# Kernel tuning notes

Measured on AMD Instinct MI355X. Metric: run time of the kernel, lower is better.

The kernel has to match this reference:

```python
import jax, jax.numpy as jnp
import numpy as np

N_NODES = 20000
N_EDGES = 320000
N_GRAPHS = 128
IN_CH = 64
DIM = 32
NEG_SLOPE = 0.2
EPS = 1e-16


def _gat_conv(x, src, dst, W, att_src, att_dst, bias, heads, ch):
    """PyG GATConv (concat=True, self-loops already included in src/dst).
    x: [N, F_in]; W: [heads*ch, F_in]; att_*: [heads, ch]; bias: [heads*ch].
    Returns [N, heads*ch]."""
    N = x.shape[0]
    h = (x @ W.T).reshape(N, heads, ch)                      # [N, H, C]
    a_src = (h * att_src[None]).sum(-1)                      # [N, H]
    a_dst = (h * att_dst[None]).sum(-1)                      # [N, H]
    e = jax.nn.leaky_relu(a_src[src] + a_dst[dst], NEG_SLOPE)  # [E, H]
    # segment softmax over edges sharing a destination node
    m = jax.ops.segment_max(e, dst, num_segments=N)          # [N, H]
    ex = jnp.exp(e - m[dst])
    s = jax.ops.segment_sum(ex, dst, num_segments=N)
    alpha = ex / (s[dst] + EPS)                              # [E, H]
    msg = alpha[:, :, None] * h[src]                         # [E, H, C]
    out = jax.ops.segment_sum(msg, dst, num_segments=N)      # [N, H, C]
    return out.reshape(N, heads * ch) + bias[None, :]


def setup_inputs() -> dict:
    key = jax.random.key(0)
    ks = jax.random.split(key, 20)

    x = jax.random.normal(ks[0], (N_NODES, IN_CH), dtype=jnp.float32)
    edge_index = jax.random.randint(ks[1], (2, N_EDGES), 0, N_NODES, dtype=jnp.int64)
    batch = jnp.sort(jax.random.randint(ks[2], (N_NODES,), 0, N_GRAPHS, dtype=jnp.int64))

    def lin_init(k, shape, fan_in):
        return jax.random.normal(k, shape, dtype=jnp.float32) * (1.0 / np.sqrt(fan_in))

    H1, C1 = 5, DIM * 2      # conv1: in -> dim*2, heads 5 -> out dim*10
    H2, C2 = 5, DIM * 3      # conv2: dim*10 -> dim*3, heads 5 -> out dim*15
    H3, C3 = 1, DIM          # conv3: dim*15 -> dim, heads 1

    inp = {
        "x": x,
        "W1": lin_init(ks[3], (H1 * C1, IN_CH), IN_CH),
        "att_src1": lin_init(ks[4], (H1, C1), C1),
        "att_dst1": lin_init(ks[5], (H1, C1), C1),
        "b1": jnp.zeros((H1 * C1,), jnp.float32),
        "W2": lin_init(ks[6], (H2 * C2, H1 * C1), H1 * C1),
        "att_src2": lin_init(ks[7], (H2, C2), C2),
        "att_dst2": lin_init(ks[8], (H2, C2), C2),
        "b2": jnp.zeros((H2 * C2,), jnp.float32),
        "W3": lin_init(ks[9], (H3 * C3, H2 * C2), H2 * C2),
        "att_src3": lin_init(ks[10], (H3, C3), C3),
        "att_dst3": lin_init(ks[11], (H3, C3), C3),
        "b3": jnp.zeros((H3 * C3,), jnp.float32),
        "lin_w": lin_init(ks[12], (1024, DIM), DIM),
        "lin_b": jnp.zeros((1024,), jnp.float32),
        "lin2_w": lin_init(ks[13], (1, 1024), 1024),
        "lin2_b": jnp.zeros((1,), jnp.float32),
        "edge_index": edge_index,
        "batch": batch,
    }
    return inp


def reference(x, W1, att_src1, att_dst1, b1,
              W2, att_src2, att_dst2, b2,
              W3, att_src3, att_dst3, b3,
              lin_w, lin_b, lin2_w, lin2_b,
              edge_index, batch):
    N = x.shape[0]
    # PyG GATConv adds self-loops by default
    loops = jnp.arange(N, dtype=edge_index.dtype)
    src = jnp.concatenate([edge_index[0], loops])
    dst = jnp.concatenate([edge_index[1], loops])

    h = _gat_conv(x, src, dst, W1, att_src1, att_dst1, b1, 5, DIM * 2)
    h = jax.nn.relu(h)                                   # dropout p=0 -> identity
    h = _gat_conv(h, src, dst, W2, att_src2, att_dst2, b2, 5, DIM * 3)
    h = jax.nn.relu(h)
    h = _gat_conv(h, src, dst, W3, att_src3, att_dst3, b3, 1, DIM)
    h = jax.nn.relu(h)

    g = jax.ops.segment_sum(h, batch, num_segments=N_GRAPHS)   # global_add_pool [G, dim]
    g = jax.nn.relu(g @ lin_w.T + lin_b[None, :])
    g = g @ lin2_w.T + lin2_b[None, :]
    return jax.nn.sigmoid(g)                                   # [G, out_channels]
```

## Files before the change

kernel.cpp:

```cpp
#include <hip/hip_runtime.h>
#include <math.h>

#define NN 20000
#define NE 320000
#define NG 128

typedef short short8 __attribute__((ext_vector_type(8)));
typedef float f32x4 __attribute__((ext_vector_type(4)));
typedef float f32x2 __attribute__((ext_vector_type(2)));
typedef unsigned short ushort;
typedef unsigned short ushort4v __attribute__((ext_vector_type(4)));
typedef float float4v __attribute__((ext_vector_type(4)));
typedef unsigned int uint;
typedef unsigned int uint2v __attribute__((ext_vector_type(2)));

__device__ __forceinline__ float b2f(ushort u) {
    unsigned int v = ((unsigned int)u) << 16;
    return __uint_as_float(v);
}
__device__ __forceinline__ ushort f2b(float f) {
    unsigned int u = __float_as_uint(f);
    u = (u + 0x7fff + ((u >> 16) & 1)) >> 16;
    return (ushort)u;
}
__device__ __forceinline__ float lrelu(float x) { return x >= 0.f ? x : 0.2f * x; }
__device__ __forceinline__ unsigned char f2f8(float v) {
    return (unsigned char)(__builtin_amdgcn_cvt_pk_fp8_f32(v, v, 0, false) & 0xff);
}
__device__ __forceinline__ void dec8(uint2v r, f32x2 d[4]) {
    d[0] = __builtin_amdgcn_cvt_pk_f32_fp8(r.x, false);
    d[1] = __builtin_amdgcn_cvt_pk_f32_fp8(r.x, true);
    d[2] = __builtin_amdgcn_cvt_pk_f32_fp8(r.y, false);
    d[3] = __builtin_amdgcn_cvt_pk_f32_fp8(r.y, true);
}

#define CVT_N0 (NN * 64 / 4)
#define CVT_N1 (320 * 64 / 4)
#define CVT_N2 (480 * 320 / 4)
#define CVT_N3 (32 * 480 / 4)
__global__ void f2b4_kernel(const float* __restrict__ a0, ushort* __restrict__ o0,
                            const float* __restrict__ a1, ushort* __restrict__ o1,
                            const float* __restrict__ a2, ushort* __restrict__ o2,
                            const float* __restrict__ a3, ushort* __restrict__ o3) {
    int i = blockIdx.x * blockDim.x + threadIdx.x;
    const float* src; ushort* dst; int li;
    if (i < CVT_N0) { src = a0; dst = o0; li = i; }
    else if (i < CVT_N0 + CVT_N1) { src = a1; dst = o1; li = i - CVT_N0; }
    else if (i < CVT_N0 + CVT_N1 + CVT_N2) { src = a2; dst = o2; li = i - CVT_N0 - CVT_N1; }
    else if (i < CVT_N0 + CVT_N1 + CVT_N2 + CVT_N3) { src = a3; dst = o3; li = i - CVT_N0 - CVT_N1 - CVT_N2; }
    else return;
    float4v v = *(const float4v*)(src + (size_t)li * 4);
    ushort4v r;
    r.x = f2b(v.x); r.y = f2b(v.y); r.z = f2b(v.z); r.w = f2b(v.w);
    *(ushort4v*)(dst + (size_t)li * 4) = r;
}

__global__ void count_kernel(const int* __restrict__ dst, int* __restrict__ cnt, int E) {
    int i = blockIdx.x * blockDim.x + threadIdx.x;
    if (i < E) atomicAdd(&cnt[dst[i]], 1);
}

__global__ __launch_bounds__(1024) void scan_kernel(const int* __restrict__ cnt,
                                                    int* __restrict__ row_start, int n) {
    __shared__ int sh[1024];
    int tid = threadIdx.x;
    int base = tid * 20;
    int local[20];
    int s = 0;
    #pragma unroll
    for (int k = 0; k < 20; ++k) {
        int idx = base + k;
        int v = (idx < n) ? cnt[idx] : 0;
        local[k] = s;
        s += v;
    }
    sh[tid] = s;
    __syncthreads();
    for (int off = 1; off < 1024; off <<= 1) {
        int t = (tid >= off) ? sh[tid - off] : 0;
        __syncthreads();
        sh[tid] += t;
        __syncthreads();
    }
    int pre = (tid == 0) ? 0 : sh[tid - 1];
    #pragma unroll
    for (int k = 0; k < 20; ++k) {
        int idx = base + k;
        if (idx < n) row_start[idx] = pre + local[k];
    }
    if (tid == 1023) row_start[n] = sh[1023];
}

__global__ void fill_kernel(const int* __restrict__ src, const int* __restrict__ dst,
                            const int* __restrict__ row_start, int* __restrict__ cursor,
                            int* __restrict__ csr_src, int E) {
    int i = blockIdx.x * blockDim.x + threadIdx.x;
    if (i < E) {
        int d = dst[i];
        int pos = atomicAdd(&cursor[d], 1);
        csr_src[row_start[d] + pos] = src[i];
    }
}

template <int K, int NF, int H, bool F8>
__global__ __launch_bounds__(256) void gemm_lds(const ushort* __restrict__ A,
                                                const ushort* __restrict__ B,
                                                ushort* __restrict__ C,
                                                unsigned char* __restrict__ C8,
                                                const float* __restrict__ att_src,
                                                const float* __restrict__ att_dst,
                                                float* __restrict__ a_src,
                                                float* __restrict__ a_dst,
                                                int M, int N, int gridx) {
    constexpr int BN = NF * 16;
    constexpr int KP = K + 8;
    constexpr int KS = K / 32;
    __shared__ ushort Bs[BN][KP];

    const int nwg = gridDim.x;
    int bid = blockIdx.x;
    {
        int q = nwg >> 3, r = nwg & 7;
        int xcd = bid & 7, idx = bid >> 3;
        bid = (xcd < r ? xcd * (q + 1) : r * (q + 1) + (xcd - r) * q) + idx;
    }
    const int by = bid / gridx;
    const int bx = bid % gridx;
    const int bn = bx * BN;

    const int tid = threadIdx.x;
    const int w = tid >> 6;
    const int lane = tid & 63;
    const int l15 = lane & 15;
    const int lhi = lane >> 4;

    constexpr int NCH = BN * (K / 8);
    for (int i = tid; i < NCH; i += 256) {
        int r = i / (K / 8), c8 = i % (K / 8);
        short8 v = *(const short8*)(B + (size_t)(bn + r) * K + c8 * 8);
        *(short8*)(&Bs[r][c8 * 8]) = v;
    }
    __syncthreads();

    const int bm = by * 64 + w * 16;
    int arow = bm + l15;
    if (arow >= M) arow = M - 1;
    const ushort* ap = A + (size_t)arow * K + lhi * 8;

    f32x4 acc[NF];
    #pragma unroll
    for (int f = 0; f < NF; ++f) acc[f] = (f32x4){0.f, 0.f, 0.f, 0.f};

    short8 a_cur = *(const short8*)ap;
    short8 b_cur[NF], b_nxt[NF];
    #pragma unroll
    for (int f = 0; f < NF; ++f)
        b_cur[f] = *(const short8*)(&Bs[f * 16 + l15][lhi * 8]);

    #pragma unroll
    for (int ks = 0; ks < KS; ++ks) {
        short8 a_nxt = a_cur;
        if (ks + 1 < KS) {
            a_nxt = *(const short8*)(ap + (ks + 1) * 32);
            #pragma unroll
            for (int f = 0; f < NF; ++f)
                b_nxt[f] = *(const short8*)(&Bs[f * 16 + l15][(ks + 1) * 32 + lhi * 8]);
        }
        #pragma unroll
        for (int f = 0; f < NF; ++f)
            acc[f] = __builtin_amdgcn_mfma_f32_16x16x32_bf16(a_cur, b_cur[f], acc[f], 0, 0, 0);
        a_cur = a_nxt;
        #pragma unroll
        for (int f = 0; f < NF; ++f) b_cur[f] = b_nxt[f];
    }

    #pragma unroll
    for (int f = 0; f < NF; ++f) {
        #pragma unroll
        for (int j = 0; j < 4; ++j) {
            int row = bm + lhi * 4 + j;
            if (row < M) {
                if (F8) C8[(size_t)row * N + bn + f * 16 + l15] = f2f8(acc[f][j]);
                else    C[(size_t)row * N + bn + f * 16 + l15] = f2b(acc[f][j]);
            }
        }
    }

    float as_v[NF], ad_v[NF];
    #pragma unroll
    for (int f = 0; f < NF; ++f) {
        as_v[f] = att_src[bx * BN + f * 16 + l15];
        ad_v[f] = att_dst[bx * BN + f * 16 + l15];
    }
    #pragma unroll
    for (int j = 0; j < 4; ++j) {
        float ps = 0.f, pd = 0.f;
        #pragma unroll
        for (int f = 0; f < NF; ++f) {
            ps += acc[f][j] * as_v[f];
            pd += acc[f][j] * ad_v[f];
        }
        #pragma unroll
        for (int off = 1; off < 16; off <<= 1) {
            ps += __shfl_xor(ps, off);
            pd += __shfl_xor(pd, off);
        }
        int row = bm + lhi * 4 + j;
        if (l15 == 0 && row < M) {
            a_src[row * H + bx] = ps;
            a_dst[row * H + bx] = pd;
        }
    }
}

template <int H, int C>
__global__ void gat_agg_f8(const unsigned char* __restrict__ h8,
                           const float* __restrict__ a_src, const float* __restrict__ a_dst,
                           const int* __restrict__ row_start, const int* __restrict__ csr_src,
                           const float* __restrict__ bias, ushort* __restrict__ out, int N) {
    constexpr int W = H * C;
    constexpr int VL = W / 8;
    int n = (blockIdx.x * blockDim.x + threadIdx.x) >> 6;
    int lane = threadIdx.x & 63;
    if (n >= N) return;
    bool act = lane < VL;
    int l = act ? lane : 0;
    int hd = (8 * l) / C;
    float adst = a_dst[n * H + hd];

    float m = lrelu(a_src[n * H + hd] + adst);
    float ssum = 1.f;
    f32x2 acc2[4];
    {
        uint2v r = *(const uint2v*)(h8 + (size_t)n * W + 8 * l);
        dec8(r, acc2);
    }

    int rs = row_start[n], re = row_start[n + 1];
    int i = rs;
    for (; i + 4 <= re; i += 4) {
        int s0 = csr_src[i], s1 = csr_src[i + 1], s2 = csr_src[i + 2], s3 = csr_src[i + 3];
        uint2v r0 = *(const uint2v*)(h8 + (size_t)s0 * W + 8 * l);
        uint2v r1 = *(const uint2v*)(h8 + (size_t)s1 * W + 8 * l);
        uint2v r2 = *(const uint2v*)(h8 + (size_t)s2 * W + 8 * l);
        uint2v r3 = *(const uint2v*)(h8 + (size_t)s3 * W + 8 * l);
        float e0 = lrelu(a_src[s0 * H + hd] + adst);
        float e1 = lrelu(a_src[s1 * H + hd] + adst);
        float e2 = lrelu(a_src[s2 * H + hd] + adst);
        float e3 = lrelu(a_src[s3 * H + hd] + adst);
        float nm = fmaxf(fmaxf(fmaxf(e0, e1), fmaxf(e2, e3)), m);
        float scale = __expf(m - nm);
        m = nm;
        float w0 = __expf(e0 - m), w1 = __expf(e1 - m);
        float w2 = __expf(e2 - m), w3 = __expf(e3 - m);
        ssum = ssum * scale + ((w0 + w1) + (w2 + w3));
        f32x2 d0[4], d1[4], d2[4], d3[4];
        dec8(r0, d0); dec8(r1, d1); dec8(r2, d2); dec8(r3, d3);
        f32x2 sc = {scale, scale};
        f32x2 vw0 = {w0, w0}, vw1 = {w1, w1}, vw2 = {w2, w2}, vw3 = {w3, w3};
        #pragma unroll
        for (int d = 0; d < 4; ++d) {
            f32x2 t = acc2[d] * sc;
            t += vw0 * d0[d];
            t += vw1 * d1[d];
            t += vw2 * d2[d];
            t += vw3 * d3[d];
            acc2[d] = t;
        }
    }
    for (; i < re; ++i) {
        int s = csr_src[i];
        uint2v r = *(const uint2v*)(h8 + (size_t)s * W + 8 * l);
        float e = lrelu(a_src[s * H + hd] + adst);
        float nm = fmaxf(m, e);
        float scale = __expf(m - nm);
        m = nm;
        float wgt = __expf(e - nm);
        ssum = ssum * scale + wgt;
        f32x2 dd[4];
        dec8(r, dd);
        f32x2 sc = {scale, scale};
        f32x2 vw = {wgt, wgt};
        #pragma unroll
        for (int d = 0; d < 4; ++d) acc2[d] = acc2[d] * sc + vw * dd[d];
    }

    float inv = 1.f / (ssum + 1e-16f);
    if (act) {
        short8 o;
        #pragma unroll
        for (int d = 0; d < 4; ++d) {
            #pragma unroll
            for (int e = 0; e < 2; ++e) {
                float v = acc2[d][e] * inv + bias[8 * l + 2 * d + e];
                o[2 * d + e] = (short)f2b(v > 0.f ? v : 0.f);
            }
        }
        *(short8*)(out + (size_t)n * W + 8 * l) = o;
    }
}

__global__ void gat_agg_c32(const ushort* __restrict__ h, const float* __restrict__ a_src,
                            const float* __restrict__ a_dst, const int* __restrict__ row_start,
                            const int* __restrict__ csr_src, const float* __restrict__ bias,
                            ushort* __restrict__ out, int N) {
    int n = (blockIdx.x * blockDim.x + threadIdx.x) >> 6;
    int lane = threadIdx.x & 63;
    if (n >= N) return;
    int g = lane >> 2;
    int q = lane & 3;
    float adst = a_dst[n];
    int rs = row_start[n];
    int total = row_start[n + 1] - rs + 1;

    float m = -1e30f, ssum = 0.f;
    float acc[8];
    #pragma unroll
    for (int j = 0; j < 8; ++j) acc[j] = 0.f;

    for (int k = g; k < total; k += 16) {
        int s = (k == 0) ? n : csr_src[rs + k - 1];
        float e = lrelu(a_src[s] + adst);
        float nm = fmaxf(m, e);
        float scale = __expf(m - nm);
        m = nm;
        float w = __expf(e - nm);
        ssum = ssum * scale + w;
        short8 r = *(const short8*)(h + (size_t)s * 32 + 8 * q);
        #pragma unroll
        for (int j = 0; j < 8; ++j) acc[j] = acc[j] * scale + w * b2f((ushort)r[j]);
    }

    #pragma unroll
    for (int off = 4; off < 64; off <<= 1) {
        float m2 = __shfl_xor(m, off);
        float s2 = __shfl_xor(ssum, off);
        float nm = fmaxf(m, m2);
        float sc1 = __expf(m - nm), sc2 = __expf(m2 - nm);
        ssum = ssum * sc1 + s2 * sc2;
        #pragma unroll
        for (int j = 0; j < 8; ++j) {
            float a2 = __shfl_xor(acc[j], off);
            acc[j] = acc[j] * sc1 + a2 * sc2;
        }
        m = nm;
    }

    if (lane < 4) {
        float inv = 1.f / (ssum + 1e-16f);
        short8 o;
        #pragma unroll
        for (int j = 0; j < 8; ++j) {
            float v = acc[j] * inv + bias[8 * lane + j];
            o[j] = (short)f2b(v > 0.f ? v : 0.f);
        }
        *(short8*)(out + (size_t)n * 32 + 8 * lane) = o;
    }
}

__global__ void pool_kernel(const ushort* __restrict__ x, const int* __restrict__ batch,
                            float* __restrict__ g, int N) {
    int wid = (blockIdx.x * blockDim.x + threadIdx.x) >> 6;
    int lane = threadIdx.x & 63;
    int node = wid * 2 + (lane >> 5);
    if (node >= N) return;
    int c = lane & 31;
    int b = batch[node];
    atomicAdd(&g[b * 32 + c], b2f(x[(size_t)node * 32 + c]));
}

__global__ void mlp1_kernel(const float* __restrict__ g, const float* __restrict__ w,
                            const float* __restrict__ b, float* __restrict__ hid) {
    int idx = blockIdx.x * blockDim.x + threadIdx.x;
    if (idx >= NG * 1024) return;
    int gr = idx >> 10, o = idx & 1023;
    float s = b[o];
    const float* gp = g + gr * 32;
    const float* wp = w + o * 32;
    #pragma unroll
    for (int k = 0; k < 32; ++k) s += gp[k] * wp[k];
    hid[idx] = s > 0.f ? s : 0.f;
}

__global__ void mlp2_kernel(const float* __restrict__ hid, const float* __restrict__ w2,
                            const float* __restrict__ b2, float* __restrict__ outp) {
    int wid = (blockIdx.x * blockDim.x + threadIdx.x) >> 6;
    int lane = threadIdx.x & 63;
    if (wid >= NG) return;
    float s = 0.f;
    for (int k = lane; k < 1024; k += 64) s += hid[wid * 1024 + k] * w2[k];
    for (int off = 32; off; off >>= 1) s += __shfl_down(s, off);
    if (lane == 0) outp[wid] = 1.f / (1.f + expf(-(s + b2[0])));
}

static inline size_t al256(size_t x) { return (x + 255) & ~(size_t)255; }

extern "C" void kernel_launch(void* const* d_in, const int* in_sizes, int n_in,
                              void* d_out, int out_size, void* d_ws, size_t ws_size,
                              hipStream_t stream) {
    const float* x      = (const float*)d_in[0];
    const float* W1     = (const float*)d_in[1];
    const float* as1    = (const float*)d_in[2];
    const float* ad1    = (const float*)d_in[3];
    const float* b1     = (const float*)d_in[4];
    const float* W2     = (const float*)d_in[5];
    const float* as2    = (const float*)d_in[6];
    const float* ad2    = (const float*)d_in[7];
    const float* b2     = (const float*)d_in[8];
    const float* W3     = (const float*)d_in[9];
    const float* as3    = (const float*)d_in[10];
    const float* ad3    = (const float*)d_in[11];
    const float* b3     = (const float*)d_in[12];
    const float* lin_w  = (const float*)d_in[13];
    const float* lin_b  = (const float*)d_in[14];
    const float* lin2_w = (const float*)d_in[15];
    const float* lin2_b = (const float*)d_in[16];
    const int*   ei     = (const int*)d_in[17];
    const int*   batch  = (const int*)d_in[18];
    float* outp = (float*)d_out;

    const int E = in_sizes[17] / 2;
    const int* e_src = ei;
    const int* e_dst = ei + E;

    char* p = (char*)d_ws;
    ushort* h_bf   = (ushort*)p; p += al256((size_t)NN * 480 * 2);
    ushort* o_bf   = (ushort*)p; p += al256((size_t)NN * 480 * 2);
    unsigned char* h_f8 = (unsigned char*)p; p += al256((size_t)NN * 480);
    ushort* x_bf   = (ushort*)p; p += al256((size_t)NN * 64 * 2);
    ushort* w1_bf  = (ushort*)p; p += al256((size_t)320 * 64 * 2);
    ushort* w2_bf  = (ushort*)p; p += al256((size_t)480 * 320 * 2);
    ushort* w3_bf  = (ushort*)p; p += al256((size_t)32 * 480 * 2);
    float* asrc    = (float*)p; p += al256((size_t)NN * 5 * 4);
    float* adst    = (float*)p; p += al256((size_t)NN * 5 * 4);
    int*   row_st  = (int*)p;   p += al256((size_t)(NN + 1) * 4);
    int*   cnt     = (int*)p;   p += al256((size_t)NN * 4);
    int*   csr_src = (int*)p;   p += al256((size_t)NE * 4);
    float* gpool   = (float*)p; p += al256((size_t)NG * 32 * 4);
    float* hidden  = (float*)p; p += al256((size_t)NG * 1024 * 4);
    (void)ws_size; (void)n_in; (void)out_size;

    dim3 blk(256);

    hipMemsetAsync(cnt, 0, NN * 4, stream);
    count_kernel<<<(E + 255) / 256, 256, 0, stream>>>(e_dst, cnt, E);
    scan_kernel<<<1, 1024, 0, stream>>>(cnt, row_st, NN);
    hipMemsetAsync(cnt, 0, NN * 4, stream);
    fill_kernel<<<(E + 255) / 256, 256, 0, stream>>>(e_src, e_dst, row_st, cnt, csr_src, E);

    {
        int tot = CVT_N0 + CVT_N1 + CVT_N2 + CVT_N3;
        f2b4_kernel<<<(tot + 255) / 256, blk, 0, stream>>>(x, x_bf, W1, w1_bf, W2, w2_bf, W3, w3_bf);
    }

    const int MPAN = (NN + 63) / 64;
    const int NBLK = (NN + 3) / 4;
    {
        gemm_lds<64, 4, 5, true><<<5 * MPAN, blk, 0, stream>>>(x_bf, w1_bf, h_bf, h_f8, as1, ad1, asrc, adst, NN, 320, 5);
        gat_agg_f8<5, 64><<<NBLK, blk, 0, stream>>>(h_f8, asrc, adst, row_st, csr_src, b1, o_bf, NN);
    }
    {
        gemm_lds<320, 6, 5, true><<<5 * MPAN, blk, 0, stream>>>(o_bf, w2_bf, h_bf, h_f8, as2, ad2, asrc, adst, NN, 480, 5);
        gat_agg_f8<5, 96><<<NBLK, blk, 0, stream>>>(h_f8, asrc, adst, row_st, csr_src, b2, o_bf, NN);
    }
    {
        gemm_lds<480, 2, 1, false><<<1 * MPAN, blk, 0, stream>>>(o_bf, w3_bf, h_bf, h_f8, as3, ad3, asrc, adst, NN, 32, 1);
        gat_agg_c32<<<NBLK, blk, 0, stream>>>(h_bf, asrc, adst, row_st, csr_src, b3, o_bf, NN);
    }
    hipMemsetAsync(gpool, 0, NG * 32 * 4, stream);
    pool_kernel<<<(NN / 2 * 64 + 255) / 256, blk, 0, stream>>>(o_bf, batch, gpool, NN);
    mlp1_kernel<<<(NG * 1024 + 255) / 256, blk, 0, stream>>>(gpool, lin_w, lin_b, hidden);
    mlp2_kernel<<<(NG * 64 + 255) / 256, blk, 0, stream>>>(hidden, lin2_w, lin2_b, outp);
}
```

Measured before the change: 212.1 us.

## Fuse pooling into last aggregation, merge MLP kernels, chunk GEMM B tiles

```diff
diff --git a/kernel.cpp b/kernel.cpp
--- a/kernel.cpp
+++ b/kernel.cpp
@@ -41,8 +41,13 @@
 __global__ void f2b4_kernel(const float* __restrict__ a0, ushort* __restrict__ o0,
                             const float* __restrict__ a1, ushort* __restrict__ o1,
                             const float* __restrict__ a2, ushort* __restrict__ o2,
-                            const float* __restrict__ a3, ushort* __restrict__ o3) {
+                            const float* __restrict__ a3, ushort* __restrict__ o3,
+                            float* __restrict__ gpool) {
     int i = blockIdx.x * blockDim.x + threadIdx.x;
+    if (i < NG * 32 / 4) {
+        float4v z = {0.f, 0.f, 0.f, 0.f};
+        *(float4v*)(gpool + (size_t)i * 4) = z;
+    }
     const float* src; ushort* dst; int li;
     if (i < CVT_N0) { src = a0; dst = o0; li = i; }
     else if (i < CVT_N0 + CVT_N1) { src = a1; dst = o1; li = i - CVT_N0; }
@@ -113,9 +118,10 @@
                                                 float* __restrict__ a_dst,
                                                 int M, int N, int gridx) {
     constexpr int BN = NF * 16;
-    constexpr int KP = K + 8;
-    constexpr int KS = K / 32;
-    __shared__ ushort Bs[BN][KP];
+    constexpr int KC = (K % 160 == 0) ? 160 : K;
+    constexpr int NCHK = K / KC;
+    constexpr int KS = KC / 32;
+    __shared__ ushort Bs[BN][KC + 8];
 
     const int nwg = gridDim.x;
     int bid = blockIdx.x;
@@ -134,14 +140,6 @@
     const int l15 = lane & 15;
     const int lhi = lane >> 4;
 
-    constexpr int NCH = BN * (K / 8);
-    for (int i = tid; i < NCH; i += 256) {
-        int r = i / (K / 8), c8 = i % (K / 8);
-        short8 v = *(const short8*)(B + (size_t)(bn + r) * K + c8 * 8);
-        *(short8*)(&Bs[r][c8 * 8]) = v;
-    }
-    __syncthreads();
-
     const int bm = by * 64 + w * 16;
     int arow = bm + l15;
     if (arow >= M) arow = M - 1;
@@ -151,27 +149,40 @@
     #pragma unroll
     for (int f = 0; f < NF; ++f) acc[f] = (f32x4){0.f, 0.f, 0.f, 0.f};
 
-    short8 a_cur = *(const short8*)ap;
-    short8 b_cur[NF], b_nxt[NF];
-    #pragma unroll
-    for (int f = 0; f < NF; ++f)
-        b_cur[f] = *(const short8*)(&Bs[f * 16 + l15][lhi * 8]);
-
-    #pragma unroll
-    for (int ks = 0; ks < KS; ++ks) {
-        short8 a_nxt = a_cur;
-        if (ks + 1 < KS) {
-            a_nxt = *(const short8*)(ap + (ks + 1) * 32);
+    #pragma unroll
+    for (int ch = 0; ch < NCHK; ++ch) {
+        const int c0 = ch * KC;
+        if (ch > 0) __syncthreads();
+        constexpr int NCH = BN * (KC / 8);
+        for (int i = tid; i < NCH; i += 256) {
+            int r = i / (KC / 8), c8 = i % (KC / 8);
+            short8 v = *(const short8*)(B + (size_t)(bn + r) * K + c0 + c8 * 8);
+            *(short8*)(&Bs[r][c8 * 8]) = v;
+        }
+        __syncthreads();
+
+        short8 a_cur = *(const short8*)(ap + c0);
+        short8 b_cur[NF], b_nxt[NF];
+        #pragma unroll
+        for (int f = 0; f < NF; ++f)
+            b_cur[f] = *(const short8*)(&Bs[f * 16 + l15][lhi * 8]);
+
+        #pragma unroll
+        for (int ks = 0; ks < KS; ++ks) {
+            short8 a_nxt = a_cur;
+            if (ks + 1 < KS) {
+                a_nxt = *(const short8*)(ap + c0 + (ks + 1) * 32);
+                #pragma unroll
+                for (int f = 0; f < NF; ++f)
+                    b_nxt[f] = *(const short8*)(&Bs[f * 16 + l15][(ks + 1) * 32 + lhi * 8]);
+            }
             #pragma unroll
             for (int f = 0; f < NF; ++f)
-                b_nxt[f] = *(const short8*)(&Bs[f * 16 + l15][(ks + 1) * 32 + lhi * 8]);
-        }
-        #pragma unroll
-        for (int f = 0; f < NF; ++f)
-            acc[f] = __builtin_amdgcn_mfma_f32_16x16x32_bf16(a_cur, b_cur[f], acc[f], 0, 0, 0);
-        a_cur = a_nxt;
-        #pragma unroll
-        for (int f = 0; f < NF; ++f) b_cur[f] = b_nxt[f];
+                acc[f] = __builtin_amdgcn_mfma_f32_16x16x32_bf16(a_cur, b_cur[f], acc[f], 0, 0, 0);
+            a_cur = a_nxt;
+            #pragma unroll
+            for (int f = 0; f < NF; ++f) b_cur[f] = b_nxt[f];
+        }
     }
 
     #pragma unroll
@@ -238,35 +249,65 @@
 
     int rs = row_start[n], re = row_start[n + 1];
     int i = rs;
-    for (; i + 4 <= re; i += 4) {
-        int s0 = csr_src[i], s1 = csr_src[i + 1], s2 = csr_src[i + 2], s3 = csr_src[i + 3];
-        uint2v r0 = *(const uint2v*)(h8 + (size_t)s0 * W + 8 * l);
-        uint2v r1 = *(const uint2v*)(h8 + (size_t)s1 * W + 8 * l);
-        uint2v r2 = *(const uint2v*)(h8 + (size_t)s2 * W + 8 * l);
-        uint2v r3 = *(const uint2v*)(h8 + (size_t)s3 * W + 8 * l);
-        float e0 = lrelu(a_src[s0 * H + hd] + adst);
-        float e1 = lrelu(a_src[s1 * H + hd] + adst);
-        float e2 = lrelu(a_src[s2 * H + hd] + adst);
-        float e3 = lrelu(a_src[s3 * H + hd] + adst);
-        float nm = fmaxf(fmaxf(fmaxf(e0, e1), fmaxf(e2, e3)), m);
+    for (; i + 8 <= re; i += 8) {
+        int s[8]; uint2v r[8]; float e[8];
+        #pragma unroll
+        for (int j = 0; j < 8; ++j) s[j] = csr_src[i + j];
+        #pragma unroll
+        for (int j = 0; j < 8; ++j) r[j] = *(const uint2v*)(h8 + (size_t)s[j] * W + 8 * l);
+        #pragma unroll
+        for (int j = 0; j < 8; ++j) e[j] = lrelu(a_src[s[j] * H + hd] + adst);
+        float nm = m;
+        #pragma unroll
+        for (int j = 0; j < 8; ++j) nm = fmaxf(nm, e[j]);
         float scale = __expf(m - nm);
         m = nm;
-        float w0 = __expf(e0 - m), w1 = __expf(e1 - m);
-        float w2 = __expf(e2 - m), w3 = __expf(e3 - m);
-        ssum = ssum * scale + ((w0 + w1) + (w2 + w3));
-        f32x2 d0[4], d1[4], d2[4], d3[4];
-        dec8(r0, d0); dec8(r1, d1); dec8(r2, d2); dec8(r3, d3);
         f32x2 sc = {scale, scale};
-        f32x2 vw0 = {w0, w0}, vw1 = {w1, w1}, vw2 = {w2, w2}, vw3 = {w3, w3};
-        #pragma unroll
-        for (int d = 0; d < 4; ++d) {
-            f32x2 t = acc2[d] * sc;
-            t += vw0 * d0[d];
-            t += vw1 * d1[d];
-            t += vw2 * d2[d];
-            t += vw3 * d3[d];
-            acc2[d] = t;
-        }
+        #pragma unroll
+        for (int d = 0; d < 4; ++d) acc2[d] *= sc;
+        ssum *= scale;
+        float wsum = 0.f;
+        #pragma unroll
+        for (int j = 0; j < 8; ++j) {
+            float wj = __expf(e[j] - nm);
+            wsum += wj;
+            f32x2 dd[4];
+            dec8(r[j], dd);
+            f32x2 vw = {wj, wj};
+            #pragma unroll
+            for (int d = 0; d < 4; ++d) acc2[d] += vw * dd[d];
+        }
+        ssum += wsum;
+    }
+    for (; i + 4 <= re; i += 4) {
+        int s[4]; uint2v r[4]; float e[4];
+        #pragma unroll
+        for (int j = 0; j < 4; ++j) s[j] = csr_src[i + j];
+        #pragma unroll
+        for (int j = 0; j < 4; ++j) r[j] = *(const uint2v*)(h8 + (size_t)s[j] * W + 8 * l);
+        #pragma unroll
+        for (int j = 0; j < 4; ++j) e[j] = lrelu(a_src[s[j] * H + hd] + adst);
+        float nm = m;
+        #pragma unroll
+        for (int j = 0; j < 4; ++j) nm = fmaxf(nm, e[j]);
+        float scale = __expf(m - nm);
+        m = nm;
+        f32x2 sc = {scale, scale};
+        #pragma unroll
+        for (int d = 0; d < 4; ++d) acc2[d] *= sc;
+        ssum *= scale;
+        float wsum = 0.f;
+        #pragma unroll
+        for (int j = 0; j < 4; ++j) {
+            float wj = __expf(e[j] - nm);
+            wsum += wj;
+            f32x2 dd[4];
+            dec8(r[j], dd);
+            f32x2 vw = {wj, wj};
+            #pragma unroll
+            for (int d = 0; d < 4; ++d) acc2[d] += vw * dd[d];
+        }
+        ssum += wsum;
     }
     for (; i < re; ++i) {
         int s = csr_src[i];
@@ -291,19 +332,19 @@
         #pragma unroll
         for (int d = 0; d < 4; ++d) {
             #pragma unroll
-            for (int e = 0; e < 2; ++e) {
-                float v = acc2[d][e] * inv + bias[8 * l + 2 * d + e];
-                o[2 * d + e] = (short)f2b(v > 0.f ? v : 0.f);
+            for (int e2 = 0; e2 < 2; ++e2) {
+                float v = acc2[d][e2] * inv + bias[8 * l + 2 * d + e2];
+                o[2 * d + e2] = (short)f2b(v > 0.f ? v : 0.f);
             }
         }
         *(short8*)(out + (size_t)n * W + 8 * l) = o;
     }
 }
 
-__global__ void gat_agg_c32(const ushort* __restrict__ h, const float* __restrict__ a_src,
-                            const float* __restrict__ a_dst, const int* __restrict__ row_start,
-                            const int* __restrict__ csr_src, const float* __restrict__ bias,
-                            ushort* __restrict__ out, int N) {
+__global__ void gat_agg_c32_pool(const ushort* __restrict__ h, const float* __restrict__ a_src,
+                                 const float* __restrict__ a_dst, const int* __restrict__ row_start,
+                                 const int* __restrict__ csr_src, const float* __restrict__ bias,
+                                 const int* __restrict__ batch, float* __restrict__ gpool, int N) {
     int n = (blockIdx.x * blockDim.x + threadIdx.x) >> 6;
     int lane = threadIdx.x & 63;
     if (n >= N) return;
@@ -348,49 +389,51 @@
 
     if (lane < 4) {
         float inv = 1.f / (ssum + 1e-16f);
-        short8 o;
+        int b = batch[n];
         #pragma unroll
         for (int j = 0; j < 8; ++j) {
             float v = acc[j] * inv + bias[8 * lane + j];
-            o[j] = (short)f2b(v > 0.f ? v : 0.f);
-        }
-        *(short8*)(out + (size_t)n * 32 + 8 * lane) = o;
-    }
-}
-
-__global__ void pool_kernel(const ushort* __restrict__ x, const int* __restrict__ batch,
-                            float* __restrict__ g, int N) {
-    int wid = (blockIdx.x * blockDim.x + threadIdx.x) >> 6;
-    int lane = threadIdx.x & 63;
-    int node = wid * 2 + (lane >> 5);
-    if (node >= N) return;
-    int c = lane & 31;
-    int b = batch[node];
-    atomicAdd(&g[b * 32 + c], b2f(x[(size_t)node * 32 + c]));
-}
-
-__global__ void mlp1_kernel(const float* __restrict__ g, const float* __restrict__ w,
-                            const float* __restrict__ b, float* __restrict__ hid) {
-    int idx = blockIdx.x * blockDim.x + threadIdx.x;
-    if (idx >= NG * 1024) return;
-    int gr = idx >> 10, o = idx & 1023;
-    float s = b[o];
-    const float* gp = g + gr * 32;
-    const float* wp = w + o * 32;
-    #pragma unroll
-    for (int k = 0; k < 32; ++k) s += gp[k] * wp[k];
-    hid[idx] = s > 0.f ? s : 0.f;
-}
-
-__global__ void mlp2_kernel(const float* __restrict__ hid, const float* __restrict__ w2,
-                            const float* __restrict__ b2, float* __restrict__ outp) {
-    int wid = (blockIdx.x * blockDim.x + threadIdx.x) >> 6;
-    int lane = threadIdx.x & 63;
-    if (wid >= NG) return;
-    float s = 0.f;
-    for (int k = lane; k < 1024; k += 64) s += hid[wid * 1024 + k] * w2[k];
-    for (int off = 32; off; off >>= 1) s += __shfl_down(s, off);
-    if (lane == 0) outp[wid] = 1.f / (1.f + expf(-(s + b2[0])));
+            v = v > 0.f ? v : 0.f;
+            atomicAdd(&gpool[b * 32 + 8 * lane + j], v);
+        }
+    }
+}
+
+__global__ __launch_bounds__(256) void mlp_fused(const float* __restrict__ gpool,
+                                                 const float* __restrict__ lin_w,
+                                                 const float* __restrict__ lin_b,
+                                                 const float* __restrict__ lin2_w,
+                                                 const float* __restrict__ lin2_b,
+                                                 float* __restrict__ outp) {
+    int gr = blockIdx.x;
+    int tid = threadIdx.x;
+    __shared__ float grow[32];
+    __shared__ float red[4];
+    if (tid < 8) {
+        float4v v = *(const float4v*)(gpool + gr * 32 + tid * 4);
+        *(float4v*)(&grow[tid * 4]) = v;
+    }
+    __syncthreads();
+    float partial = 0.f;
+    #pragma unroll
+    for (int u = 0; u < 4; ++u) {
+        int o = tid + u * 256;
+        float s = lin_b[o];
+        const float* wp = lin_w + (size_t)o * 32;
+        #pragma unroll
+        for (int k = 0; k < 32; ++k) s += grow[k] * wp[k];
+        s = s > 0.f ? s : 0.f;
+        partial += s * lin2_w[o];
+    }
+    #pragma unroll
+    for (int off = 32; off; off >>= 1) partial += __shfl_down(partial, off);
+    int lane = tid & 63, wv = tid >> 6;
+    if (lane == 0) red[wv] = partial;
+    __syncthreads();
+    if (tid == 0) {
+        float t = red[0] + red[1] + red[2] + red[3] + lin2_b[0];
+        outp[gr] = 1.f / (1.f + expf(-t));
+    }
 }
 
 static inline size_t al256(size_t x) { return (x + 255) & ~(size_t)255; }
@@ -434,23 +477,23 @@
     float* asrc    = (float*)p; p += al256((size_t)NN * 5 * 4);
     float* adst    = (float*)p; p += al256((size_t)NN * 5 * 4);
     int*   row_st  = (int*)p;   p += al256((size_t)(NN + 1) * 4);
-    int*   cnt     = (int*)p;   p += al256((size_t)NN * 4);
+    int*   cnt     = (int*)p;   p += (size_t)NN * 4;
+    int*   cursor  = (int*)p;   p += (size_t)NN * 4;
+    p = (char*)al256((size_t)p);
     int*   csr_src = (int*)p;   p += al256((size_t)NE * 4);
     float* gpool   = (float*)p; p += al256((size_t)NG * 32 * 4);
-    float* hidden  = (float*)p; p += al256((size_t)NG * 1024 * 4);
     (void)ws_size; (void)n_in; (void)out_size;
 
     dim3 blk(256);
 
-    hipMemsetAsync(cnt, 0, NN * 4, stream);
+    hipMemsetAsync(cnt, 0, (size_t)2 * NN * 4, stream);
     count_kernel<<<(E + 255) / 256, 256, 0, stream>>>(e_dst, cnt, E);
     scan_kernel<<<1, 1024, 0, stream>>>(cnt, row_st, NN);
-    hipMemsetAsync(cnt, 0, NN * 4, stream);
-    fill_kernel<<<(E + 255) / 256, 256, 0, stream>>>(e_src, e_dst, row_st, cnt, csr_src, E);
+    fill_kernel<<<(E + 255) / 256, 256, 0, stream>>>(e_src, e_dst, row_st, cursor, csr_src, E);
 
     {
         int tot = CVT_N0 + CVT_N1 + CVT_N2 + CVT_N3;
-        f2b4_kernel<<<(tot + 255) / 256, blk, 0, stream>>>(x, x_bf, W1, w1_bf, W2, w2_bf, W3, w3_bf);
+        f2b4_kernel<<<(tot + 255) / 256, blk, 0, stream>>>(x, x_bf, W1, w1_bf, W2, w2_bf, W3, w3_bf, gpool);
     }
 
     const int MPAN = (NN + 63) / 64;
@@ -465,10 +508,7 @@
     }
     {
         gemm_lds<480, 2, 1, false><<<1 * MPAN, blk, 0, stream>>>(o_bf, w3_bf, h_bf, h_f8, as3, ad3, asrc, adst, NN, 32, 1);
-        gat_agg_c32<<<NBLK, blk, 0, stream>>>(h_bf, asrc, adst, row_st, csr_src, b3, o_bf, NN);
-    }
-    hipMemsetAsync(gpool, 0, NG * 32 * 4, stream);
-    pool_kernel<<<(NN / 2 * 64 + 255) / 256, blk, 0, stream>>>(o_bf, batch, gpool, NN);
-    mlp1_kernel<<<(NG * 1024 + 255) / 256, blk, 0, stream>>>(gpool, lin_w, lin_b, hidden);
-    mlp2_kernel<<<(NG * 64 + 255) / 256, blk, 0, stream>>>(hidden, lin2_w, lin2_b, outp);
-}
+        gat_agg_c32_pool<<<NBLK, blk, 0, stream>>>(h_bf, asrc, adst, row_st, csr_src, b3, batch, gpool, NN);
+    }
+    mlp_fused<<<NG, blk, 0, stream>>>(gpool, lin_w, lin_b, lin2_w, lin2_b, outp);
+}
```

After: 255.6 us. +20.5%, slower.
